# Performance work log

Hardware: AMD Instinct MI355X
Metric: run time of the kernel (lower is better)

The kernel has to match this reference:

```python
import jax, jax.numpy as jnp
import numpy as np

N_NODES = 100000
N_EDGES = 1600000
IN_DIM = 128
HID = 256
OUT_DIM = 1
NUM_GRAPHS = 2048


def setup_inputs() -> dict:
    key = jax.random.key(0)
    ks = jax.random.split(key, 12)
    x = jax.random.normal(ks[0], (N_NODES, IN_DIM), dtype=jnp.float32)
    edge_index = jax.random.randint(ks[1], (2, N_EDGES), 0, N_NODES, dtype=jnp.int32)
    batch = jnp.sort(jax.random.randint(ks[2], (N_NODES,), 0, NUM_GRAPHS, dtype=jnp.int32))
    def glorot(k, shape):
        lim = float(np.sqrt(6.0 / (shape[0] + shape[1])))
        return jax.random.uniform(k, shape, jnp.float32, -lim, lim)
    W1 = glorot(ks[3], (IN_DIM, HID));  b1 = jnp.zeros((HID,), jnp.float32)
    W2 = glorot(ks[4], (HID, HID));     b2 = jnp.zeros((HID,), jnp.float32)
    Wf1 = glorot(ks[5], (HID, HID // 2)); bf1 = jnp.zeros((HID // 2,), jnp.float32)
    Wf2 = glorot(ks[6], (HID // 2, OUT_DIM)); bf2 = jnp.zeros((OUT_DIM,), jnp.float32)
    return {"x": x, "edge_index": edge_index, "batch": batch,
            "W1": W1, "b1": b1, "W2": W2, "b2": b2,
            "Wf1": Wf1, "bf1": bf1, "Wf2": Wf2, "bf2": bf2}


def _gcn_conv(x, W, b, src, dst, norm, num_nodes):
    # PyG GCNConv: h = X W; out[dst] += norm_e * h[src]; out += b
    h = x @ W                                   # [N, F]
    msg = h[src] * norm[:, None]                # [E', F] gather + scale
    agg = jax.ops.segment_sum(msg, dst, num_segments=num_nodes)
    return agg + b


def reference(x, edge_index, batch, W1, b1, W2, b2, Wf1, bf1, Wf2, bf2):
    n = x.shape[0]
    loop = jnp.arange(n, dtype=edge_index.dtype)
    src = jnp.concatenate([edge_index[0], loop])  # add self-loops (GCN default)
    dst = jnp.concatenate([edge_index[1], loop])
    # symmetric normalization: deg over A+I at dst index
    deg = jax.ops.segment_sum(jnp.ones_like(src, dtype=x.dtype), dst, num_segments=n)
    dinv = jnp.where(deg > 0, jax.lax.rsqrt(deg), 0.0)
    norm = dinv[src] * dinv[dst]                 # [E']

    h = jax.nn.relu(_gcn_conv(x, W1, b1, src, dst, norm, n))
    h = jax.nn.relu(_gcn_conv(h, W2, b2, src, dst, norm, n))

    # global_mean_pool over graphs
    sums = jax.ops.segment_sum(h, batch, num_segments=NUM_GRAPHS)
    cnts = jax.ops.segment_sum(jnp.ones((n,), h.dtype), batch, num_segments=NUM_GRAPHS)
    pooled = sums / jnp.maximum(cnts, 1.0)[:, None]   # [G, HID]

    out = jax.nn.relu(pooled @ Wf1 + bf1) @ Wf2 + bf2  # [G, OUT_DIM]
    return out
```

## Files before the change

### kernel.cpp

```cpp
#include <hip/hip_runtime.h>
#include <hip/hip_bf16.h>

#define N_NODES 100000
#define N_EDGES 1600000
#define IN_DIM 128
#define HID 256
#define NUM_GRAPHS 2048
#define M_PAD 100096
#define SCAN_BLOCKS 98

typedef __bf16 bf16x8 __attribute__((ext_vector_type(8)));
typedef float f32x4 __attribute__((ext_vector_type(4)));

__device__ inline unsigned short f2bf(float x) {
    union { __hip_bfloat16 h; unsigned short u; } v;
    v.h = __float2bfloat16(x);
    return v.u;
}
__device__ inline float bf2f(unsigned short u) {
    return __uint_as_float(((unsigned int)u) << 16);
}

__global__ void count_deg_kernel(const int* __restrict__ ei, int* __restrict__ deg) {
    int e = blockIdx.x * blockDim.x + threadIdx.x;
    if (e < N_EDGES) {
        atomicAdd(&deg[ei[N_EDGES + e]], 1);
    }
}

__global__ __launch_bounds__(1024) void blocksum_kernel(const int* __restrict__ deg,
                                                        int* __restrict__ bsum,
                                                        float* __restrict__ dinv) {
    int i = blockIdx.x * 1024 + threadIdx.x;
    int v = (i < N_NODES) ? deg[i] : 0;
    if (i < N_NODES) dinv[i] = rsqrtf((float)(v + 1));
    __shared__ int s[1024];
    int t = threadIdx.x;
    s[t] = v;
    __syncthreads();
#pragma unroll
    for (int off = 512; off > 0; off >>= 1) {
        if (t < off) s[t] += s[t + off];
        __syncthreads();
    }
    if (t == 0) bsum[blockIdx.x] = s[0];
}

__global__ __launch_bounds__(128) void bscan_kernel(int* __restrict__ bsum) {
    __shared__ int s[128];
    int t = threadIdx.x;
    int v = (t < SCAN_BLOCKS) ? bsum[t] : 0;
    s[t] = v;
    __syncthreads();
#pragma unroll
    for (int off = 1; off < 128; off <<= 1) {
        int x = (t >= off) ? s[t - off] : 0;
        __syncthreads();
        s[t] += x;
        __syncthreads();
    }
    if (t < SCAN_BLOCKS) bsum[t] = (t > 0) ? s[t - 1] : 0;
}

__global__ __launch_bounds__(1024) void scanout_kernel(const int* __restrict__ deg,
                                                       const int* __restrict__ bsum,
                                                       int* __restrict__ rowptr) {
    int i = blockIdx.x * 1024 + threadIdx.x;
    int t = threadIdx.x;
    int v = (i < N_NODES) ? deg[i] : 0;
    __shared__ int s[1024];
    s[t] = v;
    __syncthreads();
#pragma unroll
    for (int off = 1; off < 1024; off <<= 1) {
        int x = (t >= off) ? s[t - off] : 0;
        __syncthreads();
        s[t] += x;
        __syncthreads();
    }
    int base = bsum[blockIdx.x];
    int excl = (t > 0) ? s[t - 1] : 0;
    if (i < N_NODES) rowptr[i] = base + excl;
    if (i == N_NODES - 1) rowptr[N_NODES] = base + s[t];
}

__global__ void fill_kernel(const int* __restrict__ ei, const int* __restrict__ rowptr,
                            int* __restrict__ fill, int* __restrict__ esrc) {
    int e = blockIdx.x * blockDim.x + threadIdx.x;
    if (e < N_EDGES) {
        int dst = ei[N_EDGES + e];
        int pos = rowptr[dst] + atomicAdd(&fill[dst], 1);
        esrc[pos] = ei[e];
    }
}

__global__ void x2bf_kernel(const float* __restrict__ x, unsigned short* __restrict__ xb) {
    size_t i = ((size_t)blockIdx.x * 256 + threadIdx.x) * 4;
    float4 v = *(const float4*)(x + i);
    ushort4 o;
    o.x = f2bf(v.x); o.y = f2bf(v.y); o.z = f2bf(v.z); o.w = f2bf(v.w);
    *(ushort4*)(xb + i) = o;
}

__global__ void wsplit_all_kernel(const float* __restrict__ W1, const float* __restrict__ W2,
                                  unsigned short* __restrict__ W1th, unsigned short* __restrict__ W1tl,
                                  unsigned short* __restrict__ W2th, unsigned short* __restrict__ W2tl) {
    int idx = blockIdx.x * 256 + threadIdx.x;
    if (idx < IN_DIM * 256) {
        int k = idx >> 8, n = idx & 255;
        float w = W1[idx];
        unsigned short h = f2bf(w);
        unsigned short l = f2bf(w - bf2f(h));
        W1th[n * IN_DIM + k] = h;
        W1tl[n * IN_DIM + k] = l;
    } else {
        int i2 = idx - IN_DIM * 256;
        int k = i2 >> 8, n = i2 & 255;
        float w = W2[i2];
        unsigned short h = f2bf(w);
        unsigned short l = f2bf(w - bf2f(h));
        W2th[n * HID + k] = h;
        W2tl[n * HID + k] = l;
    }
}

__global__ __launch_bounds__(256) void agg128_kernel(const unsigned short* __restrict__ X,
                                                     const int* __restrict__ esrc,
                                                     const int* __restrict__ rowptr,
                                                     const float* __restrict__ dinv,
                                                     unsigned short* __restrict__ Ah,
                                                     unsigned short* __restrict__ Al) {
    int node = __builtin_amdgcn_readfirstlane(blockIdx.x * 4 + (threadIdx.x >> 6));
    int lane = threadIdx.x & 63;
    float ddst = dinv[node];
    int s = __builtin_amdgcn_readfirstlane(rowptr[node]);
    int e = __builtin_amdgcn_readfirstlane(rowptr[node + 1]);

    float w0 = ddst * ddst;
    ushort2 h0 = *((const ushort2*)(X + (size_t)node * 128) + lane);
    float2 acc = make_float2(w0 * bf2f(h0.x), w0 * bf2f(h0.y));

    int j = s;
    for (; j + 8 <= e; j += 8) {
        int si[8];
#pragma unroll
        for (int u = 0; u < 8; u++) si[u] = __builtin_amdgcn_readfirstlane(esrc[j + u]);
        ushort2 xv[8];
#pragma unroll
        for (int u = 0; u < 8; u++)
            xv[u] = *((const ushort2*)(X + (size_t)si[u] * 128) + lane);
        float a[8];
#pragma unroll
        for (int u = 0; u < 8; u++) a[u] = dinv[si[u]] * ddst;
#pragma unroll
        for (int u = 0; u < 8; u++) {
            acc.x = fmaf(a[u], bf2f(xv[u].x), acc.x);
            acc.y = fmaf(a[u], bf2f(xv[u].y), acc.y);
        }
    }
    for (; j + 4 <= e; j += 4) {
        int si[4];
#pragma unroll
        for (int u = 0; u < 4; u++) si[u] = __builtin_amdgcn_readfirstlane(esrc[j + u]);
        ushort2 xv[4];
#pragma unroll
        for (int u = 0; u < 4; u++)
            xv[u] = *((const ushort2*)(X + (size_t)si[u] * 128) + lane);
        float a[4];
#pragma unroll
        for (int u = 0; u < 4; u++) a[u] = dinv[si[u]] * ddst;
#pragma unroll
        for (int u = 0; u < 4; u++) {
            acc.x = fmaf(a[u], bf2f(xv[u].x), acc.x);
            acc.y = fmaf(a[u], bf2f(xv[u].y), acc.y);
        }
    }
    for (; j < e; j++) {
        int src = __builtin_amdgcn_readfirstlane(esrc[j]);
        float w = dinv[src] * ddst;
        ushort2 xv = *((const ushort2*)(X + (size_t)src * 128) + lane);
        acc.x = fmaf(w, bf2f(xv.x), acc.x);
        acc.y = fmaf(w, bf2f(xv.y), acc.y);
    }
    size_t o = (size_t)node * 128 + lane * 2;
    ushort2 hi, lo;
    hi.x = f2bf(acc.x); lo.x = f2bf(acc.x - bf2f(hi.x));
    hi.y = f2bf(acc.y); lo.y = f2bf(acc.y - bf2f(hi.y));
    *(ushort2*)(Ah + o) = hi;
    *(ushort2*)(Al + o) = lo;
}

__global__ __launch_bounds__(256) void agg256_kernel(const unsigned short* __restrict__ H,
                                                     const int* __restrict__ esrc,
                                                     const int* __restrict__ rowptr,
                                                     const float* __restrict__ dinv,
                                                     unsigned short* __restrict__ Ah) {
    int node = __builtin_amdgcn_readfirstlane(blockIdx.x * 4 + (threadIdx.x >> 6));
    int lane = threadIdx.x & 63;
    float ddst = dinv[node];
    int s = __builtin_amdgcn_readfirstlane(rowptr[node]);
    int e = __builtin_amdgcn_readfirstlane(rowptr[node + 1]);

    float w0 = ddst * ddst;
    ushort4 h0 = *((const ushort4*)(H + (size_t)node * 256) + lane);
    float4 acc = make_float4(w0 * bf2f(h0.x), w0 * bf2f(h0.y),
                             w0 * bf2f(h0.z), w0 * bf2f(h0.w));

    int j = s;
    for (; j + 8 <= e; j += 8) {
        int si[8];
#pragma unroll
        for (int u = 0; u < 8; u++) si[u] = __builtin_amdgcn_readfirstlane(esrc[j + u]);
        ushort4 xv[8];
#pragma unroll
        for (int u = 0; u < 8; u++)
            xv[u] = *((const ushort4*)(H + (size_t)si[u] * 256) + lane);
        float a[8];
#pragma unroll
        for (int u = 0; u < 8; u++) a[u] = dinv[si[u]] * ddst;
#pragma unroll
        for (int u = 0; u < 8; u++) {
            acc.x = fmaf(a[u], bf2f(xv[u].x), acc.x);
            acc.y = fmaf(a[u], bf2f(xv[u].y), acc.y);
            acc.z = fmaf(a[u], bf2f(xv[u].z), acc.z);
            acc.w = fmaf(a[u], bf2f(xv[u].w), acc.w);
        }
    }
    for (; j + 4 <= e; j += 4) {
        int si[4];
#pragma unroll
        for (int u = 0; u < 4; u++) si[u] = __builtin_amdgcn_readfirstlane(esrc[j + u]);
        ushort4 xv[4];
#pragma unroll
        for (int u = 0; u < 4; u++)
            xv[u] = *((const ushort4*)(H + (size_t)si[u] * 256) + lane);
        float a[4];
#pragma unroll
        for (int u = 0; u < 4; u++) a[u] = dinv[si[u]] * ddst;
#pragma unroll
        for (int u = 0; u < 4; u++) {
            acc.x = fmaf(a[u], bf2f(xv[u].x), acc.x);
            acc.y = fmaf(a[u], bf2f(xv[u].y), acc.y);
            acc.z = fmaf(a[u], bf2f(xv[u].z), acc.z);
            acc.w = fmaf(a[u], bf2f(xv[u].w), acc.w);
        }
    }
    for (; j < e; j++) {
        int src = __builtin_amdgcn_readfirstlane(esrc[j]);
        float w = dinv[src] * ddst;
        ushort4 xv = *((const ushort4*)(H + (size_t)src * 256) + lane);
        acc.x = fmaf(w, bf2f(xv.x), acc.x);
        acc.y = fmaf(w, bf2f(xv.y), acc.y);
        acc.z = fmaf(w, bf2f(xv.z), acc.z);
        acc.w = fmaf(w, bf2f(xv.w), acc.w);
    }
    size_t o = (size_t)node * 256 + lane * 4;
    ushort4 hi;
    hi.x = f2bf(acc.x); hi.y = f2bf(acc.y);
    hi.z = f2bf(acc.z); hi.w = f2bf(acc.w);
    *(ushort4*)(Ah + o) = hi;
}

template <int K, bool ASPLIT>
__launch_bounds__(256, 2)
__global__ void mfma_gemm_bias_relu(const unsigned short* __restrict__ Ah,
                                    const unsigned short* __restrict__ Al,
                                    const unsigned short* __restrict__ Bh,
                                    const unsigned short* __restrict__ Bl,
                                    const float* __restrict__ bias,
                                    unsigned short* __restrict__ Cout) {
    constexpr int NT = ASPLIT ? 4 : 3;
    __shared__ __align__(16) unsigned short lds[NT * 128 * 32];
    unsigned short* Ahs = lds;
    unsigned short* Als = lds + 4096;
    unsigned short* Bhs = lds + (ASPLIT ? 8192 : 4096);
    unsigned short* Bls = lds + (ASPLIT ? 12288 : 8192);

    int tid = threadIdx.x;
    int bm = blockIdx.x * 128;
    int bn = blockIdx.y * 128;
    int wid = tid >> 6, lane = tid & 63;
    int wm = wid & 1, wn = wid >> 1;
    int lrow = lane & 15, quad = lane >> 4;

    f32x4 acc[4][4];
#pragma unroll
    for (int mi = 0; mi < 4; mi++)
#pragma unroll
        for (int ni = 0; ni < 4; ni++) acc[mi][ni] = (f32x4){0.f, 0.f, 0.f, 0.f};

    for (int k0 = 0; k0 < K; k0 += 32) {
#pragma unroll
        for (int i = 0; i < NT * 2; i++) {
            int c = tid + 256 * i;
            int tile = c >> 9;
            int w = c & 511;
            int row = w >> 2;
            int part = w & 3;
            const unsigned short* g;
            if (ASPLIT) {
                if (tile == 0)      g = Ah + (size_t)(bm + row) * K + k0 + part * 8;
                else if (tile == 1) g = Al + (size_t)(bm + row) * K + k0 + part * 8;
                else if (tile == 2) g = Bh + (size_t)(bn + row) * K + k0 + part * 8;
                else                g = Bl + (size_t)(bn + row) * K + k0 + part * 8;
            } else {
                if (tile == 0)      g = Ah + (size_t)(bm + row) * K + k0 + part * 8;
                else if (tile == 1) g = Bh + (size_t)(bn + row) * K + k0 + part * 8;
                else                g = Bl + (size_t)(bn + row) * K + k0 + part * 8;
            }
            ulonglong2 v = *(const ulonglong2*)g;
            *(ulonglong2*)&lds[(tile << 12) + row * 32 + part * 8] = v;
        }
        __syncthreads();

        bf16x8 ah[4], al[4], bh[4], bl[4];
#pragma unroll
        for (int mi = 0; mi < 4; mi++) {
            int r = wm * 64 + mi * 16 + lrow;
            ah[mi] = *(const bf16x8*)&Ahs[r * 32 + quad * 8];
            if (ASPLIT) al[mi] = *(const bf16x8*)&Als[r * 32 + quad * 8];
        }
#pragma unroll
        for (int ni = 0; ni < 4; ni++) {
            int r = wn * 64 + ni * 16 + lrow;
            bh[ni] = *(const bf16x8*)&Bhs[r * 32 + quad * 8];
            bl[ni] = *(const bf16x8*)&Bls[r * 32 + quad * 8];
        }
#pragma unroll
        for (int mi = 0; mi < 4; mi++)
#pragma unroll
            for (int ni = 0; ni < 4; ni++) {
                acc[mi][ni] = __builtin_amdgcn_mfma_f32_16x16x32_bf16(ah[mi], bh[ni], acc[mi][ni], 0, 0, 0);
                acc[mi][ni] = __builtin_amdgcn_mfma_f32_16x16x32_bf16(ah[mi], bl[ni], acc[mi][ni], 0, 0, 0);
                if (ASPLIT)
                    acc[mi][ni] = __builtin_amdgcn_mfma_f32_16x16x32_bf16(al[mi], bh[ni], acc[mi][ni], 0, 0, 0);
            }
        __syncthreads();
    }

    float bv[4];
#pragma unroll
    for (int ni = 0; ni < 4; ni++) bv[ni] = bias[bn + wn * 64 + ni * 16 + lrow];
#pragma unroll
    for (int mi = 0; mi < 4; mi++) {
        int row0 = bm + wm * 64 + mi * 16 + quad * 4;
#pragma unroll
        for (int ni = 0; ni < 4; ni++) {
            int col = bn + wn * 64 + ni * 16 + lrow;
#pragma unroll
            for (int r = 0; r < 4; r++) {
                int row = row0 + r;
                if (row < N_NODES) {
                    float v = fmaxf(acc[mi][ni][r] + bv[ni], 0.f);
                    Cout[(size_t)row * 256 + col] = f2bf(v);
                }
            }
        }
    }
}

__global__ __launch_bounds__(256) void pool_mlp_kernel(const unsigned short* __restrict__ h,
                                                       const int* __restrict__ batch,
                                                       const float* __restrict__ Wf1,
                                                       const float* __restrict__ bf1,
                                                       const float* __restrict__ Wf2,
                                                       const float* __restrict__ bf2,
                                                       float* __restrict__ out) {
    int g = blockIdx.x;
    int t = threadIdx.x;
    __shared__ int bounds[2];
    if (t < 2) {
        int target = g + t;
        int lo = 0, hi = N_NODES;
        while (lo < hi) {
            int mid = (lo + hi) >> 1;
            if (batch[mid] < target) lo = mid + 1;
            else hi = mid;
        }
        bounds[t] = lo;
    }
    __syncthreads();
    int lo = bounds[0], hi = bounds[1];

    float acc = 0.f;
    for (int n = lo; n < hi; n++) acc += bf2f(h[(size_t)n * HID + t]);
    float inv = (hi > lo) ? 1.0f / (float)(hi - lo) : 0.f;
    __shared__ float p[256];
    p[t] = acc * inv;
    __syncthreads();

    float hv = 0.f;
    if (t < 128) {
        float a = bf1[t];
#pragma unroll 8
        for (int k = 0; k < 256; k++) a = fmaf(p[k], Wf1[k * 128 + t], a);
        hv = fmaxf(a, 0.f) * Wf2[t];
    }
#pragma unroll
    for (int off = 32; off > 0; off >>= 1) hv += __shfl_down(hv, off, 64);
    __shared__ float partial[4];
    if ((t & 63) == 0) partial[t >> 6] = hv;
    __syncthreads();
    if (t == 0) out[g] = partial[0] + partial[1] + bf2[0];
}

extern "C" void kernel_launch(void* const* d_in, const int* in_sizes, int n_in,
                              void* d_out, int out_size, void* d_ws, size_t ws_size,
                              hipStream_t stream) {
    const float* x   = (const float*)d_in[0];
    const int*   ei  = (const int*)d_in[1];
    const int*   bat = (const int*)d_in[2];
    const float* W1  = (const float*)d_in[3];
    const float* b1  = (const float*)d_in[4];
    const float* W2  = (const float*)d_in[5];
    const float* b2  = (const float*)d_in[6];
    const float* Wf1 = (const float*)d_in[7];
    const float* bf1 = (const float*)d_in[8];
    const float* Wf2 = (const float*)d_in[9];
    const float* bf2 = (const float*)d_in[10];
    float* out = (float*)d_out;

    char* ws = (char*)d_ws;
    int*   deg    = (int*)(ws);
    float* dinv   = (float*)(ws + 0x0080000);
    int*   rowptr = (int*)(ws + 0x0100000);
    int*   fill   = (int*)(ws + 0x0180000);
    int*   bsum   = (int*)(ws + 0x01F0000);
    int*   esrc   = (int*)(ws + 0x0200000);
    unsigned short* W1th = (unsigned short*)(ws + 0x0820000);
    unsigned short* W1tl = (unsigned short*)(ws + 0x0830000);
    unsigned short* W2th = (unsigned short*)(ws + 0x0840000);
    unsigned short* W2tl = (unsigned short*)(ws + 0x0860000);
    unsigned short* A1h  = (unsigned short*)(ws + 0x0880000);
    unsigned short* A1l  = (unsigned short*)(ws + 0x20F0000);
    unsigned short* A2   = (unsigned short*)(ws + 0x0880000);
    unsigned short* xbf  = (unsigned short*)(ws + 0x6A40000);
    unsigned short* H1bf = (unsigned short*)(ws + 0x6A40000);
    unsigned short* H2bf = (unsigned short*)(ws + 0x6A40000);
    (void)ws_size;

    hipMemsetAsync(deg, 0, (size_t)N_NODES * sizeof(int), stream);
    hipMemsetAsync(fill, 0, (size_t)N_NODES * sizeof(int), stream);

    x2bf_kernel<<<(N_NODES * IN_DIM / 4) / 256, 256, 0, stream>>>(x, xbf);
    wsplit_all_kernel<<<((IN_DIM + HID) * 256) / 256, 256, 0, stream>>>(W1, W2, W1th, W1tl, W2th, W2tl);

    count_deg_kernel<<<(N_EDGES + 255) / 256, 256, 0, stream>>>(ei, deg);
    blocksum_kernel<<<SCAN_BLOCKS, 1024, 0, stream>>>(deg, bsum, dinv);
    bscan_kernel<<<1, 128, 0, stream>>>(bsum);
    scanout_kernel<<<SCAN_BLOCKS, 1024, 0, stream>>>(deg, bsum, rowptr);
    fill_kernel<<<(N_EDGES + 255) / 256, 256, 0, stream>>>(ei, rowptr, fill, esrc);

    agg128_kernel<<<N_NODES / 4, 256, 0, stream>>>(xbf, esrc, rowptr, dinv, A1h, A1l);
    {
        dim3 grid(M_PAD / 128, 2);
        mfma_gemm_bias_relu<IN_DIM, true><<<grid, 256, 0, stream>>>(A1h, A1l, W1th, W1tl, b1, H1bf);
    }

    agg256_kernel<<<N_NODES / 4, 256, 0, stream>>>(H1bf, esrc, rowptr, dinv, A2);
    {
        dim3 grid(M_PAD / 128, 2);
        mfma_gemm_bias_relu<HID, false><<<grid, 256, 0, stream>>>(A2, nullptr, W2th, W2tl, b2, H2bf);
    }

    pool_mlp_kernel<<<NUM_GRAPHS, 256, 0, stream>>>(H2bf, bat, Wf1, bf1, Wf2, bf2, out);
}
```

Baseline: 600.7 us.

## Fuse neighbor aggregation with MFMA GEMM per 64-row tile via LDS

Merges each layer's aggregation kernel and GEMM kernel into one kernel. Each block first aggregates 64 node rows into swizzled LDS, then runs the MFMA GEMM over the full 256 output columns, reading the weights straight from global memory. This removes the round-trip of the aggregated matrix through HBM and one launch per layer. In exchange, B fragments are no longer staged in LDS, the full-K A tile sets LDS size and occupancy, and aggregation and GEMM phases within a block no longer overlap.

Result: slower. 636.8 us (+6.0%).

```diff
diff --git a/kernel.cpp b/kernel.cpp
--- a/kernel.cpp
+++ b/kernel.cpp
@@ -20,6 +20,7 @@
 __device__ inline float bf2f(unsigned short u) {
     return __uint_as_float(((unsigned int)u) << 16);
 }
+__device__ inline int rfl(int x) { return __builtin_amdgcn_readfirstlane(x); }
 
 __global__ void count_deg_kernel(const int* __restrict__ ei, int* __restrict__ deg) {
     int e = blockIdx.x * blockDim.x + threadIdx.x;
@@ -124,234 +125,203 @@
     }
 }
 
-__global__ __launch_bounds__(256) void agg128_kernel(const unsigned short* __restrict__ X,
-                                                     const int* __restrict__ esrc,
-                                                     const int* __restrict__ rowptr,
-                                                     const float* __restrict__ dinv,
-                                                     unsigned short* __restrict__ Ah,
-                                                     unsigned short* __restrict__ Al) {
-    int node = __builtin_amdgcn_readfirstlane(blockIdx.x * 4 + (threadIdx.x >> 6));
-    int lane = threadIdx.x & 63;
-    float ddst = dinv[node];
-    int s = __builtin_amdgcn_readfirstlane(rowptr[node]);
-    int e = __builtin_amdgcn_readfirstlane(rowptr[node + 1]);
-
-    float w0 = ddst * ddst;
-    ushort2 h0 = *((const ushort2*)(X + (size_t)node * 128) + lane);
-    float2 acc = make_float2(w0 * bf2f(h0.x), w0 * bf2f(h0.y));
-
-    int j = s;
-    for (; j + 8 <= e; j += 8) {
-        int si[8];
-#pragma unroll
-        for (int u = 0; u < 8; u++) si[u] = __builtin_amdgcn_readfirstlane(esrc[j + u]);
-        ushort2 xv[8];
-#pragma unroll
-        for (int u = 0; u < 8; u++)
-            xv[u] = *((const ushort2*)(X + (size_t)si[u] * 128) + lane);
-        float a[8];
-#pragma unroll
-        for (int u = 0; u < 8; u++) a[u] = dinv[si[u]] * ddst;
-#pragma unroll
-        for (int u = 0; u < 8; u++) {
-            acc.x = fmaf(a[u], bf2f(xv[u].x), acc.x);
-            acc.y = fmaf(a[u], bf2f(xv[u].y), acc.y);
+template <int K, bool ASPLIT>
+__global__ __launch_bounds__(256, 3) void fused_layer(const unsigned short* __restrict__ X,
+                                                      const int* __restrict__ esrc,
+                                                      const int* __restrict__ rowptr,
+                                                      const float* __restrict__ dinv,
+                                                      const unsigned short* __restrict__ Bh,
+                                                      const unsigned short* __restrict__ Bl,
+                                                      const float* __restrict__ bias,
+                                                      unsigned short* __restrict__ Cout) {
+    constexpr int ROWB = K * 2;
+    __shared__ __align__(16) unsigned char lds[(ASPLIT ? 2 : 1) * 64 * ROWB];
+    unsigned char* AhsB = lds;
+    unsigned char* AlsB = lds + 64 * ROWB;
+
+    int tid = threadIdx.x;
+    int wid = tid >> 6, lane = tid & 63;
+    int bm = blockIdx.x * 64;
+
+    for (int i = 0; i < 16; i++) {
+        int r = wid * 16 + i;
+        int node = rfl(bm + r);
+        if constexpr (K == 128) {
+            float2 acc = make_float2(0.f, 0.f);
+            if (node < N_NODES) {
+                float ddst = dinv[node];
+                int s = rfl(rowptr[node]);
+                int e = rfl(rowptr[node + 1]);
+                float w0 = ddst * ddst;
+                ushort2 h0 = *((const ushort2*)(X + (size_t)node * 128) + lane);
+                acc.x = w0 * bf2f(h0.x);
+                acc.y = w0 * bf2f(h0.y);
+                int j = s;
+                for (; j + 8 <= e; j += 8) {
+                    int si[8];
+#pragma unroll
+                    for (int u = 0; u < 8; u++) si[u] = rfl(esrc[j + u]);
+                    ushort2 xv[8];
+#pragma unroll
+                    for (int u = 0; u < 8; u++)
+                        xv[u] = *((const ushort2*)(X + (size_t)si[u] * 128) + lane);
+                    float a[8];
+#pragma unroll
+                    for (int u = 0; u < 8; u++) a[u] = dinv[si[u]] * ddst;
+#pragma unroll
+                    for (int u = 0; u < 8; u++) {
+                        acc.x = fmaf(a[u], bf2f(xv[u].x), acc.x);
+                        acc.y = fmaf(a[u], bf2f(xv[u].y), acc.y);
+                    }
+                }
+                for (; j + 4 <= e; j += 4) {
+                    int si[4];
+#pragma unroll
+                    for (int u = 0; u < 4; u++) si[u] = rfl(esrc[j + u]);
+                    ushort2 xv[4];
+#pragma unroll
+                    for (int u = 0; u < 4; u++)
+                        xv[u] = *((const ushort2*)(X + (size_t)si[u] * 128) + lane);
+                    float a[4];
+#pragma unroll
+                    for (int u = 0; u < 4; u++) a[u] = dinv[si[u]] * ddst;
+#pragma unroll
+                    for (int u = 0; u < 4; u++) {
+                        acc.x = fmaf(a[u], bf2f(xv[u].x), acc.x);
+                        acc.y = fmaf(a[u], bf2f(xv[u].y), acc.y);
+                    }
+                }
+                for (; j < e; j++) {
+                    int src = rfl(esrc[j]);
+                    float w = dinv[src] * ddst;
+                    ushort2 xv = *((const ushort2*)(X + (size_t)src * 128) + lane);
+                    acc.x = fmaf(w, bf2f(xv.x), acc.x);
+                    acc.y = fmaf(w, bf2f(xv.y), acc.y);
+                }
+            }
+            unsigned bo = ((unsigned)(r * 256 + lane * 4)) ^ (((unsigned)(r & 7)) << 4);
+            ushort2 hi, lo;
+            hi.x = f2bf(acc.x); lo.x = f2bf(acc.x - bf2f(hi.x));
+            hi.y = f2bf(acc.y); lo.y = f2bf(acc.y - bf2f(hi.y));
+            *(ushort2*)(AhsB + bo) = hi;
+            if (ASPLIT) *(ushort2*)(AlsB + bo) = lo;
+        } else {
+            float4 acc = make_float4(0.f, 0.f, 0.f, 0.f);
+            if (node < N_NODES) {
+                float ddst = dinv[node];
+                int s = rfl(rowptr[node]);
+                int e = rfl(rowptr[node + 1]);
+                float w0 = ddst * ddst;
+                ushort4 h0 = *((const ushort4*)(X + (size_t)node * 256) + lane);
+                acc.x = w0 * bf2f(h0.x);
+                acc.y = w0 * bf2f(h0.y);
+                acc.z = w0 * bf2f(h0.z);
+                acc.w = w0 * bf2f(h0.w);
+                int j = s;
+                for (; j + 8 <= e; j += 8) {
+                    int si[8];
+#pragma unroll
+                    for (int u = 0; u < 8; u++) si[u] = rfl(esrc[j + u]);
+                    ushort4 xv[8];
+#pragma unroll
+                    for (int u = 0; u < 8; u++)
+                        xv[u] = *((const ushort4*)(X + (size_t)si[u] * 256) + lane);
+                    float a[8];
+#pragma unroll
+                    for (int u = 0; u < 8; u++) a[u] = dinv[si[u]] * ddst;
+#pragma unroll
+                    for (int u = 0; u < 8; u++) {
+                        acc.x = fmaf(a[u], bf2f(xv[u].x), acc.x);
+                        acc.y = fmaf(a[u], bf2f(xv[u].y), acc.y);
+                        acc.z = fmaf(a[u], bf2f(xv[u].z), acc.z);
+                        acc.w = fmaf(a[u], bf2f(xv[u].w), acc.w);
+                    }
+                }
+                for (; j + 4 <= e; j += 4) {
+                    int si[4];
+#pragma unroll
+                    for (int u = 0; u < 4; u++) si[u] = rfl(esrc[j + u]);
+                    ushort4 xv[4];
+#pragma unroll
+                    for (int u = 0; u < 4; u++)
+                        xv[u] = *((const ushort4*)(X + (size_t)si[u] * 256) + lane);
+                    float a[4];
+#pragma unroll
+                    for (int u = 0; u < 4; u++) a[u] = dinv[si[u]] * ddst;
+#pragma unroll
+                    for (int u = 0; u < 4; u++) {
+                        acc.x = fmaf(a[u], bf2f(xv[u].x), acc.x);
+                        acc.y = fmaf(a[u], bf2f(xv[u].y), acc.y);
+                        acc.z = fmaf(a[u], bf2f(xv[u].z), acc.z);
+                        acc.w = fmaf(a[u], bf2f(xv[u].w), acc.w);
+                    }
+                }
+                for (; j < e; j++) {
+                    int src = rfl(esrc[j]);
+                    float w = dinv[src] * ddst;
+                    ushort4 xv = *((const ushort4*)(X + (size_t)src * 256) + lane);
+                    acc.x = fmaf(w, bf2f(xv.x), acc.x);
+                    acc.y = fmaf(w, bf2f(xv.y), acc.y);
+                    acc.z = fmaf(w, bf2f(xv.z), acc.z);
+                    acc.w = fmaf(w, bf2f(xv.w), acc.w);
+                }
+            }
+            unsigned bo = ((unsigned)(r * 512 + lane * 8)) ^ (((unsigned)(r & 7)) << 4);
+            ushort4 hi;
+            hi.x = f2bf(acc.x); hi.y = f2bf(acc.y);
+            hi.z = f2bf(acc.z); hi.w = f2bf(acc.w);
+            *(ushort4*)(AhsB + bo) = hi;
         }
     }
-    for (; j + 4 <= e; j += 4) {
-        int si[4];
-#pragma unroll
-        for (int u = 0; u < 4; u++) si[u] = __builtin_amdgcn_readfirstlane(esrc[j + u]);
-        ushort2 xv[4];
-#pragma unroll
-        for (int u = 0; u < 4; u++)
-            xv[u] = *((const ushort2*)(X + (size_t)si[u] * 128) + lane);
-        float a[4];
-#pragma unroll
-        for (int u = 0; u < 4; u++) a[u] = dinv[si[u]] * ddst;
-#pragma unroll
-        for (int u = 0; u < 4; u++) {
-            acc.x = fmaf(a[u], bf2f(xv[u].x), acc.x);
-            acc.y = fmaf(a[u], bf2f(xv[u].y), acc.y);
+    __syncthreads();
+
+    int lrow = lane & 15, quad = lane >> 4;
+    f32x4 acc[4][4];
+#pragma unroll
+    for (int mi = 0; mi < 4; mi++)
+#pragma unroll
+        for (int ni = 0; ni < 4; ni++) acc[mi][ni] = (f32x4){0.f, 0.f, 0.f, 0.f};
+
+#pragma unroll
+    for (int k0 = 0; k0 < K; k0 += 32) {
+        bf16x8 ah[4], al[4];
+#pragma unroll
+        for (int mi = 0; mi < 4; mi++) {
+            int r = mi * 16 + lrow;
+            unsigned bo = ((unsigned)(r * ROWB + (k0 + quad * 8) * 2)) ^ (((unsigned)(r & 7)) << 4);
+            ah[mi] = *(const bf16x8*)(AhsB + bo);
+            if (ASPLIT) al[mi] = *(const bf16x8*)(AlsB + bo);
         }
-    }
-    for (; j < e; j++) {
-        int src = __builtin_amdgcn_readfirstlane(esrc[j]);
-        float w = dinv[src] * ddst;
-        ushort2 xv = *((const ushort2*)(X + (size_t)src * 128) + lane);
-        acc.x = fmaf(w, bf2f(xv.x), acc.x);
-        acc.y = fmaf(w, bf2f(xv.y), acc.y);
-    }
-    size_t o = (size_t)node * 128 + lane * 2;
-    ushort2 hi, lo;
-    hi.x = f2bf(acc.x); lo.x = f2bf(acc.x - bf2f(hi.x));
-    hi.y = f2bf(acc.y); lo.y = f2bf(acc.y - bf2f(hi.y));
-    *(ushort2*)(Ah + o) = hi;
-    *(ushort2*)(Al + o) = lo;
-}
-
-__global__ __launch_bounds__(256) void agg256_kernel(const unsigned short* __restrict__ H,
-                                                     const int* __restrict__ esrc,
-                                                     const int* __restrict__ rowptr,
-                                                     const float* __restrict__ dinv,
-                                                     unsigned short* __restrict__ Ah) {
-    int node = __builtin_amdgcn_readfirstlane(blockIdx.x * 4 + (threadIdx.x >> 6));
-    int lane = threadIdx.x & 63;
-    float ddst = dinv[node];
-    int s = __builtin_amdgcn_readfirstlane(rowptr[node]);
-    int e = __builtin_amdgcn_readfirstlane(rowptr[node + 1]);
-
-    float w0 = ddst * ddst;
-    ushort4 h0 = *((const ushort4*)(H + (size_t)node * 256) + lane);
-    float4 acc = make_float4(w0 * bf2f(h0.x), w0 * bf2f(h0.y),
-                             w0 * bf2f(h0.z), w0 * bf2f(h0.w));
-
-    int j = s;
-    for (; j + 8 <= e; j += 8) {
-        int si[8];
-#pragma unroll
-        for (int u = 0; u < 8; u++) si[u] = __builtin_amdgcn_readfirstlane(esrc[j + u]);
-        ushort4 xv[8];
-#pragma unroll
-        for (int u = 0; u < 8; u++)
-            xv[u] = *((const ushort4*)(H + (size_t)si[u] * 256) + lane);
-        float a[8];
-#pragma unroll
-        for (int u = 0; u < 8; u++) a[u] = dinv[si[u]] * ddst;
-#pragma unroll
-        for (int u = 0; u < 8; u++) {
-            acc.x = fmaf(a[u], bf2f(xv[u].x), acc.x);
-            acc.y = fmaf(a[u], bf2f(xv[u].y), acc.y);
-            acc.z = fmaf(a[u], bf2f(xv[u].z), acc.z);
-            acc.w = fmaf(a[u], bf2f(xv[u].w), acc.w);
+#pragma unroll
+        for (int ni = 0; ni < 4; ni++) {
+            int rowB = wid * 64 + ni * 16 + lrow;
+            size_t gb = (size_t)rowB * K + k0 + quad * 8;
+            bf16x8 bh = *(const bf16x8*)(Bh + gb);
+            bf16x8 bl = *(const bf16x8*)(Bl + gb);
+#pragma unroll
+            for (int mi = 0; mi < 4; mi++) {
+                acc[mi][ni] = __builtin_amdgcn_mfma_f32_16x16x32_bf16(ah[mi], bh, acc[mi][ni], 0, 0, 0);
+                acc[mi][ni] = __builtin_amdgcn_mfma_f32_16x16x32_bf16(ah[mi], bl, acc[mi][ni], 0, 0, 0);
+                if (ASPLIT)
+                    acc[mi][ni] = __builtin_amdgcn_mfma_f32_16x16x32_bf16(al[mi], bh, acc[mi][ni], 0, 0, 0);
+            }
         }
     }
-    for (; j + 4 <= e; j += 4) {
-        int si[4];
-#pragma unroll
-        for (int u = 0; u < 4; u++) si[u] = __builtin_amdgcn_readfirstlane(esrc[j + u]);
-        ushort4 xv[4];
-#pragma unroll
-        for (int u = 0; u < 4; u++)
-            xv[u] = *((const ushort4*)(H + (size_t)si[u] * 256) + lane);
-        float a[4];
-#pragma unroll
-        for (int u = 0; u < 4; u++) a[u] = dinv[si[u]] * ddst;
-#pragma unroll
-        for (int u = 0; u < 4; u++) {
-            acc.x = fmaf(a[u], bf2f(xv[u].x), acc.x);
-            acc.y = fmaf(a[u], bf2f(xv[u].y), acc.y);
-            acc.z = fmaf(a[u], bf2f(xv[u].z), acc.z);
-            acc.w = fmaf(a[u], bf2f(xv[u].w), acc.w);
-        }
-    }
-    for (; j < e; j++) {
-        int src = __builtin_amdgcn_readfirstlane(esrc[j]);
-        float w = dinv[src] * ddst;
-        ushort4 xv = *((const ushort4*)(H + (size_t)src * 256) + lane);
-        acc.x = fmaf(w, bf2f(xv.x), acc.x);
-        acc.y = fmaf(w, bf2f(xv.y), acc.y);
-        acc.z = fmaf(w, bf2f(xv.z), acc.z);
-        acc.w = fmaf(w, bf2f(xv.w), acc.w);
-    }
-    size_t o = (size_t)node * 256 + lane * 4;
-    ushort4 hi;
-    hi.x = f2bf(acc.x); hi.y = f2bf(acc.y);
-    hi.z = f2bf(acc.z); hi.w = f2bf(acc.w);
-    *(ushort4*)(Ah + o) = hi;
-}
-
-template <int K, bool ASPLIT>
-__launch_bounds__(256, 2)
-__global__ void mfma_gemm_bias_relu(const unsigned short* __restrict__ Ah,
-                                    const unsigned short* __restrict__ Al,
-                                    const unsigned short* __restrict__ Bh,
-                                    const unsigned short* __restrict__ Bl,
-                                    const float* __restrict__ bias,
-                                    unsigned short* __restrict__ Cout) {
-    constexpr int NT = ASPLIT ? 4 : 3;
-    __shared__ __align__(16) unsigned short lds[NT * 128 * 32];
-    unsigned short* Ahs = lds;
-    unsigned short* Als = lds + 4096;
-    unsigned short* Bhs = lds + (ASPLIT ? 8192 : 4096);
-    unsigned short* Bls = lds + (ASPLIT ? 12288 : 8192);
-
-    int tid = threadIdx.x;
-    int bm = blockIdx.x * 128;
-    int bn = blockIdx.y * 128;
-    int wid = tid >> 6, lane = tid & 63;
-    int wm = wid & 1, wn = wid >> 1;
-    int lrow = lane & 15, quad = lane >> 4;
-
-    f32x4 acc[4][4];
-#pragma unroll
-    for (int mi = 0; mi < 4; mi++)
-#pragma unroll
-        for (int ni = 0; ni < 4; ni++) acc[mi][ni] = (f32x4){0.f, 0.f, 0.f, 0.f};
-
-    for (int k0 = 0; k0 < K; k0 += 32) {
-#pragma unroll
-        for (int i = 0; i < NT * 2; i++) {
-            int c = tid + 256 * i;
-            int tile = c >> 9;
-            int w = c & 511;
-            int row = w >> 2;
-            int part = w & 3;
-            const unsigned short* g;
-            if (ASPLIT) {
-                if (tile == 0)      g = Ah + (size_t)(bm + row) * K + k0 + part * 8;
-                else if (tile == 1) g = Al + (size_t)(bm + row) * K + k0 + part * 8;
-                else if (tile == 2) g = Bh + (size_t)(bn + row) * K + k0 + part * 8;
-                else                g = Bl + (size_t)(bn + row) * K + k0 + part * 8;
-            } else {
-                if (tile == 0)      g = Ah + (size_t)(bm + row) * K + k0 + part * 8;
-                else if (tile == 1) g = Bh + (size_t)(bn + row) * K + k0 + part * 8;
-                else                g = Bl + (size_t)(bn + row) * K + k0 + part * 8;
-            }
-            ulonglong2 v = *(const ulonglong2*)g;
-            *(ulonglong2*)&lds[(tile << 12) + row * 32 + part * 8] = v;
-        }
-        __syncthreads();
-
-        bf16x8 ah[4], al[4], bh[4], bl[4];
-#pragma unroll
-        for (int mi = 0; mi < 4; mi++) {
-            int r = wm * 64 + mi * 16 + lrow;
-            ah[mi] = *(const bf16x8*)&Ahs[r * 32 + quad * 8];
-            if (ASPLIT) al[mi] = *(const bf16x8*)&Als[r * 32 + quad * 8];
-        }
+
+    float bv[4];
+#pragma unroll
+    for (int ni = 0; ni < 4; ni++) bv[ni] = bias[wid * 64 + ni * 16 + lrow];
+#pragma unroll
+    for (int mi = 0; mi < 4; mi++) {
+        int row0 = bm + mi * 16 + quad * 4;
 #pragma unroll
         for (int ni = 0; ni < 4; ni++) {
-            int r = wn * 64 + ni * 16 + lrow;
-            bh[ni] = *(const bf16x8*)&Bhs[r * 32 + quad * 8];
-            bl[ni] = *(const bf16x8*)&Bls[r * 32 + quad * 8];
-        }
-#pragma unroll
-        for (int mi = 0; mi < 4; mi++)
-#pragma unroll
-            for (int ni = 0; ni < 4; ni++) {
-                acc[mi][ni] = __builtin_amdgcn_mfma_f32_16x16x32_bf16(ah[mi], bh[ni], acc[mi][ni], 0, 0, 0);
-                acc[mi][ni] = __builtin_amdgcn_mfma_f32_16x16x32_bf16(ah[mi], bl[ni], acc[mi][ni], 0, 0, 0);
-                if (ASPLIT)
-                    acc[mi][ni] = __builtin_amdgcn_mfma_f32_16x16x32_bf16(al[mi], bh[ni], acc[mi][ni], 0, 0, 0);
-            }
-        __syncthreads();
-    }
-
-    float bv[4];
-#pragma unroll
-    for (int ni = 0; ni < 4; ni++) bv[ni] = bias[bn + wn * 64 + ni * 16 + lrow];
-#pragma unroll
-    for (int mi = 0; mi < 4; mi++) {
-        int row0 = bm + wm * 64 + mi * 16 + quad * 4;
-#pragma unroll
-        for (int ni = 0; ni < 4; ni++) {
-            int col = bn + wn * 64 + ni * 16 + lrow;
-#pragma unroll
-            for (int r = 0; r < 4; r++) {
-                int row = row0 + r;
+            int col = wid * 64 + ni * 16 + lrow;
+#pragma unroll
+            for (int rr = 0; rr < 4; rr++) {
+                int row = row0 + rr;
                 if (row < N_NODES) {
-                    float v = fmaxf(acc[mi][ni][r] + bv[ni], 0.f);
+                    float v = fmaxf(acc[mi][ni][rr] + bv[ni], 0.f);
                     Cout[(size_t)row * 256 + col] = f2bf(v);
                 }
             }
@@ -431,12 +401,9 @@
     unsigned short* W1tl = (unsigned short*)(ws + 0x0830000);
     unsigned short* W2th = (unsigned short*)(ws + 0x0840000);
     unsigned short* W2tl = (unsigned short*)(ws + 0x0860000);
-    unsigned short* A1h  = (unsigned short*)(ws + 0x0880000);
-    unsigned short* A1l  = (unsigned short*)(ws + 0x20F0000);
-    unsigned short* A2   = (unsigned short*)(ws + 0x0880000);
-    unsigned short* xbf  = (unsigned short*)(ws + 0x6A40000);
-    unsigned short* H1bf = (unsigned short*)(ws + 0x6A40000);
-    unsigned short* H2bf = (unsigned short*)(ws + 0x6A40000);
+    unsigned short* xbf  = (unsigned short*)(ws + 0x0880000);
+    unsigned short* H1bf = (unsigned short*)(ws + 0x2100000);
+    unsigned short* H2bf = (unsigned short*)(ws + 0x5200000);
     (void)ws_size;
 
     hipMemsetAsync(deg, 0, (size_t)N_NODES * sizeof(int), stream);
@@ -451,17 +418,11 @@
     scanout_kernel<<<SCAN_BLOCKS, 1024, 0, stream>>>(deg, bsum, rowptr);
     fill_kernel<<<(N_EDGES + 255) / 256, 256, 0, stream>>>(ei, rowptr, fill, esrc);
 
-    agg128_kernel<<<N_NODES / 4, 256, 0, stream>>>(xbf, esrc, rowptr, dinv, A1h, A1l);
-    {
-        dim3 grid(M_PAD / 128, 2);
-        mfma_gemm_bias_relu<IN_DIM, true><<<grid, 256, 0, stream>>>(A1h, A1l, W1th, W1tl, b1, H1bf);
-    }
-
-    agg256_kernel<<<N_NODES / 4, 256, 0, stream>>>(H1bf, esrc, rowptr, dinv, A2);
-    {
-        dim3 grid(M_PAD / 128, 2);
-        mfma_gemm_bias_relu<HID, false><<<grid, 256, 0, stream>>>(A2, nullptr, W2th, W2tl, b2, H2bf);
-    }
+    fused_layer<IN_DIM, true><<<M_PAD / 64, 256, 0, stream>>>(xbf, esrc, rowptr, dinv,
+                                                              W1th, W1tl, b1, H1bf);
+
+    fused_layer<HID, false><<<M_PAD / 64, 256, 0, stream>>>(H1bf, esrc, rowptr, dinv,
+                                                            W2th, W2tl, b2, H2bf);
 
     pool_mlp_kernel<<<NUM_GRAPHS, 256, 0, stream>>>(H2bf, bat, Wf1, bf1, Wf2, bf2, out);
 }
```
